# Performance work log

Hardware: AMD Instinct MI355X
Metric: run time of the kernel (lower is better)

The kernel has to match this reference:

```python
import jax, jax.numpy as jnp
import numpy as np
from jax import lax

L, B, S, D, H = 2, 8, 2048, 1024, 1024
LOG_H0 = float(np.log(0.5))  # h0 = g(0) = 0.5


def _log_g(x):
    # log of g(x) = x + 0.5 if x >= 0 else sigmoid(x)
    return jnp.where(x >= 0, jnp.log(jnp.where(x >= 0, x + 0.5, 1.0)), -jax.nn.softplus(-x))


def _mingru_layer(x, Wz, bz, Wh, bh):
    # x: (B,S,D) -> (B,S,H) via log-space heinsen associative scan
    k = jnp.einsum('bsd,hd->bsh', x, Wz) + bz          # gate pre-activation
    log_z = -jax.nn.softplus(-k)                        # log sigmoid(k)
    log_coeffs = -jax.nn.softplus(k)                    # log (1 - sigmoid(k))
    pre_h = jnp.einsum('bsd,hd->bsh', x, Wh) + bh
    log_values = log_z + _log_g(pre_h)                  # log(z * h_tilde)
    Bq = x.shape[0]
    # prepend initial state: coeff 0 (log 1), value log(h0)
    log_coeffs = jnp.pad(log_coeffs, ((0, 0), (1, 0), (0, 0)))
    log_values = jnp.concatenate(
        [jnp.full((Bq, 1, log_values.shape[-1]), LOG_H0, dtype=log_values.dtype), log_values], axis=1)
    a_star = jnp.cumsum(log_coeffs, axis=1)
    log_h = a_star + lax.cumlogsumexp(log_values - a_star, axis=1)
    return jnp.exp(log_h)[:, 1:]


def setup_inputs() -> dict:
    key = jax.random.key(0)
    ks = jax.random.split(key, 5)
    stdv = 1.0 / np.sqrt(D)
    u = lambda k, shp: jax.random.uniform(k, shp, jnp.float32, -stdv, stdv)
    return {
        'x': jax.random.normal(ks[0], (B, S, D), jnp.float32),
        'Wz': u(ks[1], (L, H, D)),
        'bz': u(ks[2], (L, H)),
        'Wh': u(ks[3], (L, H, D)),
        'bh': u(ks[4], (L, H)),
    }


def reference(x, Wz, bz, Wh, bh):
    h = x
    for l in range(Wz.shape[0]):
        h = _mingru_layer(h, Wz[l], bz[l], Wh[l], bh[l])
    return h  # (B,S,H), last layer outputs
```

## Files before the change

kernel.cpp:

```cpp
#include <hip/hip_runtime.h>
#include <hip/hip_bf16.h>


#define L_ 2
#define B_ 8
#define S_ 2048
#define D_ 1024
#define H_ 1024
#define M_ (B_*S_)
#define NC 32
#define CL (S_/NC)

typedef __bf16    bf16x8 __attribute__((ext_vector_type(8)));
typedef float     f32x4  __attribute__((ext_vector_type(4)));
typedef _Float16  h2     __attribute__((ext_vector_type(2)));
typedef _Float16  h4     __attribute__((ext_vector_type(4)));

__device__ __forceinline__ ushort f2bf(float f) {
    union { __hip_bfloat16 h; ushort u; } c;
    c.h = __float2bfloat16(f);
    return c.u;
}

__device__ __forceinline__ void async16(const void* g, void* l) {
    __builtin_amdgcn_global_load_lds(
        (const __attribute__((address_space(1))) unsigned int*)g,
        (__attribute__((address_space(3))) unsigned int*)l, 16, 0, 0);
}

__global__ __launch_bounds__(256) void cast_f32_bf16(const float* __restrict__ in,
                                                     ushort* __restrict__ out, int n4) {
    int i = blockIdx.x * 256 + threadIdx.x;
    if (i >= n4) return;
    float4 v = ((const float4*)in)[i];
    ushort4 o;
    o.x = f2bf(v.x); o.y = f2bf(v.y); o.z = f2bf(v.z); o.w = f2bf(v.w);
    ((ushort4*)out)[i] = o;
}

#define SWZ(R, c) (((R) << 6) + ((((c) ^ ((R) & 7))) << 3))
#define MFMA16 __builtin_amdgcn_mfma_f32_16x16x32_bf16
#define FENCE() asm volatile("" ::: "memory")

__global__ __launch_bounds__(512, 2) void gemm_fused(const ushort* __restrict__ A,
                                                     const ushort* __restrict__ Wz,
                                                     const ushort* __restrict__ Wh,
                                                     const float* __restrict__ bz,
                                                     const float* __restrict__ bh,
                                                     h2* __restrict__ cv,
                                                     float* __restrict__ Ac,
                                                     float* __restrict__ Bc)
{
    extern __shared__ __align__(16) ushort sm[];

    const int tid  = threadIdx.x;
    const int lane = tid & 63;
    const int wave = tid >> 6;
    const int bid  = (int)blockIdx.x;
    const int xcd  = bid & 7;
    const int k8   = bid >> 3;
    const int nblk = k8 & 7;
    const int mblk = ((k8 >> 3) << 3) + xcd;
    const int m0 = mblk << 8;
    const int n0 = nblk << 7;
    const int wm = (wave >> 2) << 7;
    const int wn = (wave & 3) << 5;
    const int lrow = lane & 15;
    const int lcq  = lane >> 4;

    const int e0 = tid, e1 = tid + 512;
    const int r0 = e0 >> 3, c0 = (((e0 & 7) ^ (r0 & 7)) << 3);
    const int r1 = e1 >> 3, c1 = (((e1 & 7) ^ (r1 & 7)) << 3);
    const uint offA0  = (uint)((m0 + r0) * D_ + c0);
    const uint offA0b = (uint)((m0 + r1) * D_ + c1);
    const uint offA1  = offA0  + (uint)(128 * D_);
    const uint offA1b = offA0b + (uint)(128 * D_);
    const uint offW0  = (uint)((n0 + r0) * D_ + c0);
    const uint offW0b = (uint)((n0 + r1) * D_ + c1);
    const int dj0 = wave << 9;
    const int dj1 = 4096 + (wave << 9);

    f32x4 accz[8][2] = {};
    f32x4 acch[8][2] = {};

    async16(A  + offA0,  &sm[dj0]);
    async16(A  + offA0b, &sm[dj1]);
    async16(A  + offA1,  &sm[8192  + dj0]);
    async16(A  + offA1b, &sm[8192  + dj1]);
    async16(Wz + offW0,  &sm[16384 + dj0]);
    async16(Wz + offW0b, &sm[16384 + dj1]);
    async16(Wh + offW0,  &sm[24576 + dj0]);
    async16(Wh + offW0b, &sm[24576 + dj1]);

    #pragma unroll 2
    for (int t = 0; t < 16; ++t) {
        const int cur = (t & 1) << 15;
        const int nxt = cur ^ 32768;
        const uint kbn = (uint)((t < 15 ? t + 1 : 15) << 6);
        bf16x8 a0[4][2], a1[4][2], zf[2][2], hf[2][2];

        asm volatile("s_waitcnt vmcnt(2)" ::: "memory");
        __builtin_amdgcn_s_barrier();
        FENCE();
        #pragma unroll
        for (int mt = 0; mt < 4; ++mt)
            #pragma unroll
            for (int kk = 0; kk < 2; ++kk)
                a0[mt][kk] = *(const bf16x8*)&sm[cur + SWZ(wm + mt*16 + lrow, kk*4 + lcq)];
        #pragma unroll
        for (int nt = 0; nt < 2; ++nt)
            #pragma unroll
            for (int kk = 0; kk < 2; ++kk)
                zf[nt][kk] = *(const bf16x8*)&sm[cur + 16384 + SWZ(wn + nt*16 + lrow, kk*4 + lcq)];
        async16(A + offA0  + kbn, &sm[nxt + dj0]);
        async16(A + offA0b + kbn, &sm[nxt + dj1]);
        __builtin_amdgcn_s_setprio(1);
        #pragma unroll
        for (int kk = 0; kk < 2; ++kk)
            #pragma unroll
            for (int nt = 0; nt < 2; ++nt)
                #pragma unroll
                for (int mt = 0; mt < 4; ++mt)
                    accz[mt][nt] = MFMA16(a0[mt][kk], zf[nt][kk], accz[mt][nt], 0, 0, 0);
        __builtin_amdgcn_s_setprio(0);

        __builtin_amdgcn_s_barrier();
        FENCE();
        #pragma unroll
        for (int mt = 0; mt < 4; ++mt)
            #pragma unroll
            for (int kk = 0; kk < 2; ++kk)
                a1[mt][kk] = *(const bf16x8*)&sm[cur + SWZ(wm + 64 + mt*16 + lrow, kk*4 + lcq)];
        async16(A + offA1  + kbn, &sm[nxt + 8192 + dj0]);
        async16(A + offA1b + kbn, &sm[nxt + 8192 + dj1]);
        __builtin_amdgcn_s_setprio(1);
        #pragma unroll
        for (int kk = 0; kk < 2; ++kk)
            #pragma unroll
            for (int nt = 0; nt < 2; ++nt)
                #pragma unroll
                for (int mt = 0; mt < 4; ++mt)
                    accz[4 + mt][nt] = MFMA16(a1[mt][kk], zf[nt][kk], accz[4 + mt][nt], 0, 0, 0);
        __builtin_amdgcn_s_setprio(0);

        asm volatile("s_waitcnt vmcnt(4)" ::: "memory");
        __builtin_amdgcn_s_barrier();
        FENCE();
        #pragma unroll
        for (int nt = 0; nt < 2; ++nt)
            #pragma unroll
            for (int kk = 0; kk < 2; ++kk)
                hf[nt][kk] = *(const bf16x8*)&sm[cur + 24576 + SWZ(wn + nt*16 + lrow, kk*4 + lcq)];
        async16(Wz + offW0  + kbn, &sm[nxt + 16384 + dj0]);
        async16(Wz + offW0b + kbn, &sm[nxt + 16384 + dj1]);
        __builtin_amdgcn_s_setprio(1);
        #pragma unroll
        for (int kk = 0; kk < 2; ++kk)
            #pragma unroll
            for (int nt = 0; nt < 2; ++nt)
                #pragma unroll
                for (int mt = 0; mt < 4; ++mt)
                    acch[4 + mt][nt] = MFMA16(a1[mt][kk], hf[nt][kk], acch[4 + mt][nt], 0, 0, 0);
        __builtin_amdgcn_s_setprio(0);

        __builtin_amdgcn_s_barrier();
        FENCE();
        async16(Wh + offW0  + kbn, &sm[nxt + 24576 + dj0]);
        async16(Wh + offW0b + kbn, &sm[nxt + 24576 + dj1]);
        __builtin_amdgcn_s_setprio(1);
        #pragma unroll
        for (int kk = 0; kk < 2; ++kk)
            #pragma unroll
            for (int nt = 0; nt < 2; ++nt)
                #pragma unroll
                for (int mt = 0; mt < 4; ++mt)
                    acch[mt][nt] = MFMA16(a0[mt][kk], hf[nt][kk], acch[mt][nt], 0, 0, 0);
        __builtin_amdgcn_s_setprio(0);
    }

    asm volatile("s_waitcnt vmcnt(0)" ::: "memory");
    __syncthreads();

    float2* seg = (float2*)sm;
    const int colq = lane & 15;
    const int rowq = (lane >> 4) << 2;
    #pragma unroll
    for (int nt = 0; nt < 2; ++nt) {
        const int n = n0 + wn + nt*16 + colq;
        const float bzv = bz[n];
        const float bhv = bh[n];
        #pragma unroll
        for (int mt = 0; mt < 8; ++mt) {
            float a = 1.f, bb = 0.f;
            #pragma unroll
            for (int r = 0; r < 4; ++r) {
                const int m = m0 + wm + mt*16 + rowq + r;
                float kx = accz[mt][nt][r] + bzv;
                float p  = acch[mt][nt][r] + bhv;
                float e   = __expf(-fabsf(kx));
                float inv = 1.0f / (1.0f + e);
                float z   = (kx >= 0.f) ? inv     : e * inv;
                float c   = (kx >= 0.f) ? e * inv : inv;
                float g;
                if (p >= 0.f) g = p + 0.5f;
                else { float eg = __expf(p); g = eg / (1.0f + eg); }
                float v = z * g;
                h2 hv; hv[0] = (_Float16)c; hv[1] = (_Float16)v;
                cv[(size_t)m * H_ + n] = hv;
                bb = fmaf(c, bb, v);
                a *= c;
            }
            const int sidx = (wm >> 2) + mt*4 + (rowq >> 2);
            seg[sidx*130 + wn + nt*16 + colq] = make_float2(a, bb);
        }
    }
    __syncthreads();
    {
        const int col = tid & 127;
        const int ch  = tid >> 7;
        float a = 1.f, bb = 0.f;
        #pragma unroll
        for (int s = 0; s < 16; ++s) {
            float2 e2 = seg[(ch*16 + s)*130 + col];
            bb = fmaf(e2.x, bb, e2.y);
            a *= e2.x;
        }
        const int b     = m0 >> 11;
        const int chunk = ((m0 >> 6) & (NC - 1)) + ch;
        const int q = (b*NC + chunk)*H_ + n0 + col;
        Ac[q] = a; Bc[q] = bb;
    }
}

__global__ __launch_bounds__(256) void scan_chunk_combine(const float* __restrict__ Ac,
                                                          const float* __restrict__ Bc,
                                                          float* __restrict__ hin)
{
    int q = blockIdx.x * 256 + threadIdx.x;
    int h = q & (H_-1);
    int b = q >> 10;
    float hcur = 0.5f;
    #pragma unroll
    for (int c = 0; c < NC; ++c) {
        int idx = (b*NC + c)*H_ + h;
        hin[idx] = hcur;
        hcur = fmaf(Ac[idx], hcur, Bc[idx]);
    }
}

__global__ __launch_bounds__(256) void scan_emit(const h2* __restrict__ cv,
                                                 const float* __restrict__ hin,
                                                 float* __restrict__ outf,
                                                 ushort* __restrict__ outb,
                                                 const int write_bf16)
{
    int q = blockIdx.x * 256 + threadIdx.x;
    int hp = (q & 511) * 2;
    int c = (q >> 9) & (NC-1);
    int b = q >> 14;
    size_t base = (size_t)(b*S_ + c*CL) * H_ + hp;
    int qh = (b*NC + c)*H_ + hp;
    float h0 = hin[qh], h1 = hin[qh + 1];
    if (write_bf16) {
        #pragma unroll 4
        for (int tt = 0; tt < CL; ++tt) {
            h4 e = *(const h4*)&cv[base + (size_t)tt * H_];
            h0 = fmaf((float)e[0], h0, (float)e[1]);
            h1 = fmaf((float)e[2], h1, (float)e[3]);
            ushort2 o; o.x = f2bf(h0); o.y = f2bf(h1);
            *(ushort2*)&outb[base + (size_t)tt * H_] = o;
        }
    } else {
        #pragma unroll 4
        for (int tt = 0; tt < CL; ++tt) {
            h4 e = *(const h4*)&cv[base + (size_t)tt * H_];
            h0 = fmaf((float)e[0], h0, (float)e[1]);
            h1 = fmaf((float)e[2], h1, (float)e[3]);
            *(float2*)&outf[base + (size_t)tt * H_] = make_float2(h0, h1);
        }
    }
}

extern "C" void kernel_launch(void* const* d_in, const int* in_sizes, int n_in,
                              void* d_out, int out_size, void* d_ws, size_t ws_size,
                              hipStream_t stream)
{
    const float* x  = (const float*)d_in[0];
    const float* Wz = (const float*)d_in[1];
    const float* bz = (const float*)d_in[2];
    const float* Wh = (const float*)d_in[3];
    const float* bh = (const float*)d_in[4];
    float* out = (float*)d_out;

    static bool attr_set = false;
    if (!attr_set) {
        (void)hipFuncSetAttribute(reinterpret_cast<const void*>(gemm_fused),
                                  hipFuncAttributeMaxDynamicSharedMemorySize, 131072);
        attr_set = true;
    }

    ushort* xb  = (ushort*)d_ws;
    ushort* wzb = xb  + (size_t)M_*D_;
    ushort* whb = wzb + (size_t)L_*H_*D_;
    h2*     cv  = (h2*)(whb + (size_t)L_*H_*D_);
    float*  Ac  = (float*)(cv + (size_t)M_*H_);
    float*  Bc  = Ac + B_*NC*H_;
    float*  hin = Bc + B_*NC*H_;

    cast_f32_bf16<<<(M_*D_/4)/256, 256, 0, stream>>>(x, xb, M_*D_/4);
    cast_f32_bf16<<<(L_*H_*D_/4)/256, 256, 0, stream>>>(Wz, wzb, L_*H_*D_/4);
    cast_f32_bf16<<<(L_*H_*D_/4)/256, 256, 0, stream>>>(Wh, whb, L_*H_*D_/4);

    const int gemm_grid = (M_/256) * (H_/128);
    for (int l = 0; l < L_; ++l) {
        gemm_fused<<<gemm_grid, 512, 131072, stream>>>(xb,
                                                       wzb + (size_t)l*H_*D_,
                                                       whb + (size_t)l*H_*D_,
                                                       bz + l*H_, bh + l*H_,
                                                       cv, Ac, Bc);
        scan_chunk_combine<<<(B_*H_)/256, 256, 0, stream>>>(Ac, Bc, hin);
        scan_emit<<<(B_*NC*H_/2)/256, 256, 0, stream>>>(cv, hin, out, xb, (l == 0) ? 1 : 0);
    }
}
```

Measured before the change: 335.4 us.

## Pack 4 timesteps per 16-byte cv store and restructure GEMM barrier schedule

The GEMM epilogue now packs the (coeff, value) fp16 pairs for four consecutive timesteps into one 16-byte store, using a new cv layout grouped by four rows. scan_emit is rewritten so each thread handles one hidden unit with 16-byte loads of that layout, and it launches twice as many threads. The GEMM main loop's barriers and waitcnts are rearranged, with extra barriers and sched_barriers, so that LDS reads finish before the MFMA clusters. The intent is fewer, wider memory transactions and a more controlled interleave of loads and MFMAs. The risk is extra barrier overhead, and scan_emit output stores drop to 2 or 4 bytes per thread per timestep, which lowers store coalescing width.

```diff
diff --git a/kernel.cpp b/kernel.cpp
--- a/kernel.cpp
+++ b/kernel.cpp
@@ -14,7 +14,7 @@
 typedef __bf16    bf16x8 __attribute__((ext_vector_type(8)));
 typedef float     f32x4  __attribute__((ext_vector_type(4)));
 typedef _Float16  h2     __attribute__((ext_vector_type(2)));
-typedef _Float16  h4     __attribute__((ext_vector_type(4)));
+typedef _Float16  h8     __attribute__((ext_vector_type(8)));
 
 __device__ __forceinline__ ushort f2bf(float f) {
     union { __hip_bfloat16 h; ushort u; } c;
@@ -41,6 +41,8 @@
 #define SWZ(R, c) (((R) << 6) + ((((c) ^ ((R) & 7))) << 3))
 #define MFMA16 __builtin_amdgcn_mfma_f32_16x16x32_bf16
 #define FENCE() asm volatile("" ::: "memory")
+#define BARRIER() __builtin_amdgcn_s_barrier()
+#define SB0() __builtin_amdgcn_sched_barrier(0)
 
 __global__ __launch_bounds__(512, 2) void gemm_fused(const ushort* __restrict__ A,
                                                      const ushort* __restrict__ Wz,
@@ -91,6 +93,9 @@
     async16(Wz + offW0b, &sm[16384 + dj1]);
     async16(Wh + offW0,  &sm[24576 + dj0]);
     async16(Wh + offW0b, &sm[24576 + dj1]);
+    asm volatile("s_waitcnt vmcnt(2)" ::: "memory");
+    BARRIER();
+    FENCE();
 
     #pragma unroll 2
     for (int t = 0; t < 16; ++t) {
@@ -99,9 +104,6 @@
         const uint kbn = (uint)((t < 15 ? t + 1 : 15) << 6);
         bf16x8 a0[4][2], a1[4][2], zf[2][2], hf[2][2];
 
-        asm volatile("s_waitcnt vmcnt(2)" ::: "memory");
-        __builtin_amdgcn_s_barrier();
-        FENCE();
         #pragma unroll
         for (int mt = 0; mt < 4; ++mt)
             #pragma unroll
@@ -114,6 +116,10 @@
                 zf[nt][kk] = *(const bf16x8*)&sm[cur + 16384 + SWZ(wn + nt*16 + lrow, kk*4 + lcq)];
         async16(A + offA0  + kbn, &sm[nxt + dj0]);
         async16(A + offA0b + kbn, &sm[nxt + dj1]);
+        asm volatile("s_waitcnt lgkmcnt(8)" ::: "memory");
+        BARRIER();
+        asm volatile("s_waitcnt lgkmcnt(0)" ::: "memory");
+        SB0();
         __builtin_amdgcn_s_setprio(1);
         #pragma unroll
         for (int kk = 0; kk < 2; ++kk)
@@ -123,9 +129,9 @@
                 for (int mt = 0; mt < 4; ++mt)
                     accz[mt][nt] = MFMA16(a0[mt][kk], zf[nt][kk], accz[mt][nt], 0, 0, 0);
         __builtin_amdgcn_s_setprio(0);
-
-        __builtin_amdgcn_s_barrier();
+        BARRIER();
         FENCE();
+
         #pragma unroll
         for (int mt = 0; mt < 4; ++mt)
             #pragma unroll
@@ -133,6 +139,10 @@
                 a1[mt][kk] = *(const bf16x8*)&sm[cur + SWZ(wm + 64 + mt*16 + lrow, kk*4 + lcq)];
         async16(A + offA1  + kbn, &sm[nxt + 8192 + dj0]);
         async16(A + offA1b + kbn, &sm[nxt + 8192 + dj1]);
+        asm volatile("s_waitcnt vmcnt(4)" ::: "memory");
+        BARRIER();
+        asm volatile("s_waitcnt lgkmcnt(0)" ::: "memory");
+        SB0();
         __builtin_amdgcn_s_setprio(1);
         #pragma unroll
         for (int kk = 0; kk < 2; ++kk)
@@ -142,10 +152,9 @@
                 for (int mt = 0; mt < 4; ++mt)
                     accz[4 + mt][nt] = MFMA16(a1[mt][kk], zf[nt][kk], accz[4 + mt][nt], 0, 0, 0);
         __builtin_amdgcn_s_setprio(0);
-
-        asm volatile("s_waitcnt vmcnt(4)" ::: "memory");
-        __builtin_amdgcn_s_barrier();
+        BARRIER();
         FENCE();
+
         #pragma unroll
         for (int nt = 0; nt < 2; ++nt)
             #pragma unroll
@@ -153,6 +162,9 @@
                 hf[nt][kk] = *(const bf16x8*)&sm[cur + 24576 + SWZ(wn + nt*16 + lrow, kk*4 + lcq)];
         async16(Wz + offW0  + kbn, &sm[nxt + 16384 + dj0]);
         async16(Wz + offW0b + kbn, &sm[nxt + 16384 + dj1]);
+        BARRIER();
+        asm volatile("s_waitcnt lgkmcnt(0)" ::: "memory");
+        SB0();
         __builtin_amdgcn_s_setprio(1);
         #pragma unroll
         for (int kk = 0; kk < 2; ++kk)
@@ -162,11 +174,14 @@
                 for (int mt = 0; mt < 4; ++mt)
                     acch[4 + mt][nt] = MFMA16(a1[mt][kk], hf[nt][kk], acch[4 + mt][nt], 0, 0, 0);
         __builtin_amdgcn_s_setprio(0);
-
-        __builtin_amdgcn_s_barrier();
+        BARRIER();
         FENCE();
+
         async16(Wh + offW0  + kbn, &sm[nxt + 24576 + dj0]);
         async16(Wh + offW0b + kbn, &sm[nxt + 24576 + dj1]);
+        asm volatile("s_waitcnt vmcnt(2)" ::: "memory");
+        BARRIER();
+        SB0();
         __builtin_amdgcn_s_setprio(1);
         #pragma unroll
         for (int kk = 0; kk < 2; ++kk)
@@ -176,6 +191,8 @@
                 for (int mt = 0; mt < 4; ++mt)
                     acch[mt][nt] = MFMA16(a0[mt][kk], hf[nt][kk], acch[mt][nt], 0, 0, 0);
         __builtin_amdgcn_s_setprio(0);
+        BARRIER();
+        FENCE();
     }
 
     asm volatile("s_waitcnt vmcnt(0)" ::: "memory");
@@ -192,9 +209,9 @@
         #pragma unroll
         for (int mt = 0; mt < 8; ++mt) {
             float a = 1.f, bb = 0.f;
+            h8 pk;
             #pragma unroll
             for (int r = 0; r < 4; ++r) {
-                const int m = m0 + wm + mt*16 + rowq + r;
                 float kx = accz[mt][nt][r] + bzv;
                 float p  = acch[mt][nt][r] + bhv;
                 float e   = __expf(-fabsf(kx));
@@ -205,11 +222,13 @@
                 if (p >= 0.f) g = p + 0.5f;
                 else { float eg = __expf(p); g = eg / (1.0f + eg); }
                 float v = z * g;
-                h2 hv; hv[0] = (_Float16)c; hv[1] = (_Float16)v;
-                cv[(size_t)m * H_ + n] = hv;
+                pk[2*r]     = (_Float16)c;
+                pk[2*r + 1] = (_Float16)v;
                 bb = fmaf(c, bb, v);
                 a *= c;
             }
+            const int mb4 = (m0 + wm + mt*16 + rowq) >> 2;
+            *(h8*)&cv[((size_t)mb4 * H_ + n) * 4] = pk;
             const int sidx = (wm >> 2) + mt*4 + (rowq >> 2);
             seg[sidx*130 + wn + nt*16 + colq] = make_float2(a, bb);
         }
@@ -255,28 +274,30 @@
                                                  const int write_bf16)
 {
     int q = blockIdx.x * 256 + threadIdx.x;
-    int hp = (q & 511) * 2;
-    int c = (q >> 9) & (NC-1);
-    int b = q >> 14;
-    size_t base = (size_t)(b*S_ + c*CL) * H_ + hp;
-    int qh = (b*NC + c)*H_ + hp;
-    float h0 = hin[qh], h1 = hin[qh + 1];
+    int h = q & (H_-1);
+    int c = (q >> 10) & (NC-1);
+    int b = q >> 15;
+    const int mb = b*S_ + c*CL;
+    float hc = hin[(b*NC + c)*H_ + h];
     if (write_bf16) {
         #pragma unroll 4
-        for (int tt = 0; tt < CL; ++tt) {
-            h4 e = *(const h4*)&cv[base + (size_t)tt * H_];
-            h0 = fmaf((float)e[0], h0, (float)e[1]);
-            h1 = fmaf((float)e[2], h1, (float)e[3]);
-            ushort2 o; o.x = f2bf(h0); o.y = f2bf(h1);
-            *(ushort2*)&outb[base + (size_t)tt * H_] = o;
+        for (int j = 0; j < 16; ++j) {
+            h8 e = *(const h8*)&cv[(((size_t)(mb >> 2) + j)*H_ + h) * 4];
+            #pragma unroll
+            for (int u = 0; u < 4; ++u) {
+                hc = fmaf((float)e[2*u], hc, (float)e[2*u + 1]);
+                outb[(size_t)(mb + 4*j + u)*H_ + h] = f2bf(hc);
+            }
         }
     } else {
         #pragma unroll 4
-        for (int tt = 0; tt < CL; ++tt) {
-            h4 e = *(const h4*)&cv[base + (size_t)tt * H_];
-            h0 = fmaf((float)e[0], h0, (float)e[1]);
-            h1 = fmaf((float)e[2], h1, (float)e[3]);
-            *(float2*)&outf[base + (size_t)tt * H_] = make_float2(h0, h1);
+        for (int j = 0; j < 16; ++j) {
+            h8 e = *(const h8*)&cv[(((size_t)(mb >> 2) + j)*H_ + h) * 4];
+            #pragma unroll
+            for (int u = 0; u < 4; ++u) {
+                hc = fmaf((float)e[2*u], hc, (float)e[2*u + 1]);
+                outf[(size_t)(mb + 4*j + u)*H_ + h] = hc;
+            }
         }
     }
 }
@@ -319,6 +340,6 @@
                                                        bz + l*H_, bh + l*H_,
                                                        cv, Ac, Bc);
         scan_chunk_combine<<<(B_*H_)/256, 256, 0, stream>>>(Ac, Bc, hin);
-        scan_emit<<<(B_*NC*H_/2)/256, 256, 0, stream>>>(cv, hin, out, xb, (l == 0) ? 1 : 0);
-    }
-}
+        scan_emit<<<(B_*NC*H_)/256, 256, 0, stream>>>(cv, hin, out, xb, (l == 0) ? 1 : 0);
+    }
+}
```

Result: no change. 339.8 us (+1.3%).
